# Kernel tuning notes

Hardware: AMD Instinct MI355X
Metric: run time of the kernel (lower is better)

Reference implementation:

```python
import jax, jax.numpy as jnp
import numpy as np

N_NODES = 50000
N_EDGES = 800000
IN_DIM, HID_DIM, OUT_DIM = 128, 128, 64


def setup_inputs() -> dict:
    key = jax.random.key(0)
    ks = jax.random.split(key, 12)
    x = jax.random.normal(ks[0], (N_NODES, IN_DIM), dtype=jnp.float32)
    src = jax.random.randint(ks[1], (N_EDGES,), 0, N_NODES, dtype=jnp.int32)
    dst = jax.random.randint(ks[2], (N_EDGES,), 0, N_NODES, dtype=jnp.int32)
    def lin(k, fan_in, fan_out):
        s = 1.0 / np.sqrt(fan_in)
        kw, kb = jax.random.split(k)
        W = jax.random.uniform(kw, (fan_in, fan_out), jnp.float32, -s, s)
        b = jax.random.uniform(kb, (fan_out,), jnp.float32, -s, s)
        return W, b
    W1, b1 = lin(ks[3], IN_DIM, HID_DIM)
    W2, b2 = lin(ks[4], HID_DIM, HID_DIM)
    W3, b3 = lin(ks[5], HID_DIM, OUT_DIM)
    Wf, bf = lin(ks[6], OUT_DIM, 1)
    return {"x": x, "src": src, "dst": dst,
            "W1": W1, "b1": b1, "W2": W2, "b2": b2,
            "W3": W3, "b3": b3, "Wf": Wf, "bf": bf}


def reference(x, src, dst, W1, b1, W2, b2, W3, b3, Wf, bf):
    n = x.shape[0]
    # GCN symmetric norm with self-loops: deg = in-degree + 1 (self loop)
    ones = jnp.ones(src.shape[0], x.dtype)
    deg = jax.ops.segment_sum(ones, dst, num_segments=n) + 1.0
    dinv = jax.lax.rsqrt(deg)                       # [N]
    edge_norm = dinv[src] * dinv[dst]               # [E]
    self_norm = dinv * dinv                         # [N], self-loop weight

    def gcn(h, W, b):
        h = h @ W                                   # transform first (PyG order)
        agg = jax.ops.segment_sum(h[src] * edge_norm[:, None], dst, num_segments=n)
        agg = agg + h * self_norm[:, None]          # self-loop contribution
        return agg + b

    h = jax.nn.relu(gcn(x, W1, b1))
    h = jax.nn.relu(gcn(h, W2, b2))
    h = jax.nn.relu(gcn(h, W3, b3))
    return h @ Wf + bf                              # [N, 1] per-node scores
```

## Files before the change

### kernel.cpp

```cpp
#include <hip/hip_runtime.h>
#include <hip/hip_bf16.h>

typedef short bf16x8 __attribute__((ext_vector_type(8)));
typedef float f32x4 __attribute__((ext_vector_type(4)));
typedef _Float16 f16x2 __attribute__((ext_vector_type(2)));
typedef _Float16 f16x8v __attribute__((ext_vector_type(8)));
typedef unsigned short u16x8 __attribute__((ext_vector_type(8)));

static __device__ __forceinline__ unsigned short f2bf_rne(float f) {
    unsigned int u = __float_as_uint(f);
    u += 0x7fff + ((u >> 16) & 1);
    return (unsigned short)(u >> 16);
}
static __device__ __forceinline__ float bf2f(unsigned short h) {
    return __uint_as_float(((unsigned int)h) << 16);
}

static __device__ __forceinline__ void wsplit_one(const float* W, unsigned short* hi,
                                                  unsigned short* lo, int BN, int idx) {
    int k = idx / BN, n = idx % BN;
    float w = W[idx];
    unsigned short h = f2bf_rne(w);
    unsigned short l = f2bf_rne(w - bf2f(h));
    int CT = BN >> 4;
    int kc = k >> 5, quad = (k >> 3) & 3, j = k & 7;
    int ct = n >> 4, c = n & 15;
    int slot = (((kc * CT + ct) * 4 + quad) * 16 + c) * 8 + j;
    hi[slot] = h;
    lo[slot] = l;
}


template<int BN>
static __device__ __forceinline__ void gemm_body_f32(const float* __restrict__ A,
                        const unsigned short* __restrict__ Whi, const unsigned short* __restrict__ Wlo,
                        _Float16* __restrict__ C, int N, int blk,
                        unsigned short* AhiS, unsigned short* AloS) {
    constexpr int CT = BN / 16;
    const int tid = threadIdx.x;
    const int wave = tid >> 6;
    const int lane = tid & 63;
    const int quad = lane >> 4;
    const int c16 = lane & 15;
    const int row0 = blk * 64;

    f32x4 acc[CT];
    #pragma unroll
    for (int t = 0; t < CT; ++t) acc[t] = (f32x4){0.f, 0.f, 0.f, 0.f};

    for (int kc = 0; kc < 4; ++kc) {
        #pragma unroll
        for (int r = 0; r < 2; ++r) {
            int f4 = tid + r * 256;
            int arow = f4 >> 3;
            int c4 = f4 & 7;
            int grow = row0 + arow;
            float4 v = make_float4(0.f, 0.f, 0.f, 0.f);
            if (grow < N) v = *(const float4*)&A[(size_t)grow * 128 + kc * 32 + c4 * 4];
            unsigned short h0 = f2bf_rne(v.x), h1 = f2bf_rne(v.y), h2 = f2bf_rne(v.z), h3 = f2bf_rne(v.w);
            ushort4 hv = make_ushort4(h0, h1, h2, h3);
            ushort4 lv = make_ushort4(f2bf_rne(v.x - bf2f(h0)), f2bf_rne(v.y - bf2f(h1)),
                                      f2bf_rne(v.z - bf2f(h2)), f2bf_rne(v.w - bf2f(h3)));
            int q = c4 >> 1;
            int joff = (c4 & 1) * 4;
            int base = (q * 64 + arow) * 8 + joff;
            *(ushort4*)&AhiS[base] = hv;
            *(ushort4*)&AloS[base] = lv;
        }
        __syncthreads();

        int abase = (quad * 64 + wave * 16 + c16) * 8;
        bf16x8 ahi = *(const bf16x8*)&AhiS[abase];
        bf16x8 alo = *(const bf16x8*)&AloS[abase];

        #pragma unroll
        for (int ct = 0; ct < CT; ++ct) {
            size_t bslot = ((size_t)(kc * CT + ct) * 64 + lane) * 8;
            bf16x8 bhi = *(const bf16x8*)&Whi[bslot];
            bf16x8 blo = *(const bf16x8*)&Wlo[bslot];
            acc[ct] = __builtin_amdgcn_mfma_f32_16x16x32_bf16(ahi, bhi, acc[ct], 0, 0, 0);
            acc[ct] = __builtin_amdgcn_mfma_f32_16x16x32_bf16(ahi, blo, acc[ct], 0, 0, 0);
            acc[ct] = __builtin_amdgcn_mfma_f32_16x16x32_bf16(alo, bhi, acc[ct], 0, 0, 0);
        }
        __syncthreads();
    }

    #pragma unroll
    for (int ct = 0; ct < CT; ++ct) {
        #pragma unroll
        for (int r = 0; r < 4; ++r) {
            int grow = row0 + wave * 16 + quad * 4 + r;
            if (grow < N) C[(size_t)grow * BN + ct * 16 + c16] = (_Float16)acc[ct][r];
        }
    }
}

template<int BN>
static __device__ __forceinline__ void gemm_body_bf(const unsigned short* __restrict__ Ahi,
                        const unsigned short* __restrict__ Alo,
                        const unsigned short* __restrict__ Whi, const unsigned short* __restrict__ Wlo,
                        _Float16* __restrict__ C, int N, int blk,
                        unsigned short* AhiS, unsigned short* AloS) {
    constexpr int CT = BN / 16;
    const int tid = threadIdx.x;
    const int wave = tid >> 6;
    const int lane = tid & 63;
    const int quad = lane >> 4;
    const int c16 = lane & 15;
    const int row0 = blk * 64;
    const int arow = tid >> 2;
    const int cblk = tid & 3;
    const int grow = row0 + arow;
    const bool inb = grow < N;
    const size_t agbase = (size_t)grow * 128 + cblk * 8;
    const int sbase = (cblk * 64 + arow) * 8;

    f32x4 acc[CT];
    #pragma unroll
    for (int t = 0; t < CT; ++t) acc[t] = (f32x4){0.f, 0.f, 0.f, 0.f};

    for (int kc = 0; kc < 4; ++kc) {
        u16x8 hv = {0, 0, 0, 0, 0, 0, 0, 0};
        u16x8 lv = {0, 0, 0, 0, 0, 0, 0, 0};
        if (inb) {
            hv = *(const u16x8*)&Ahi[agbase + kc * 32];
            lv = *(const u16x8*)&Alo[agbase + kc * 32];
        }
        *(u16x8*)&AhiS[sbase] = hv;
        *(u16x8*)&AloS[sbase] = lv;
        __syncthreads();

        int abase = (quad * 64 + wave * 16 + c16) * 8;
        bf16x8 ahi = *(const bf16x8*)&AhiS[abase];
        bf16x8 alo = *(const bf16x8*)&AloS[abase];

        #pragma unroll
        for (int ct = 0; ct < CT; ++ct) {
            size_t bslot = ((size_t)(kc * CT + ct) * 64 + lane) * 8;
            bf16x8 bhi = *(const bf16x8*)&Whi[bslot];
            bf16x8 blo = *(const bf16x8*)&Wlo[bslot];
            acc[ct] = __builtin_amdgcn_mfma_f32_16x16x32_bf16(ahi, bhi, acc[ct], 0, 0, 0);
            acc[ct] = __builtin_amdgcn_mfma_f32_16x16x32_bf16(ahi, blo, acc[ct], 0, 0, 0);
            acc[ct] = __builtin_amdgcn_mfma_f32_16x16x32_bf16(alo, bhi, acc[ct], 0, 0, 0);
        }
        __syncthreads();
    }

    #pragma unroll
    for (int ct = 0; ct < CT; ++ct) {
        #pragma unroll
        for (int r = 0; r < 4; ++r) {
            int gr = row0 + wave * 16 + quad * 4 + r;
            if (gr < N) C[(size_t)gr * BN + ct * 16 + c16] = (_Float16)acc[ct][r];
        }
    }
}


__global__ __launch_bounds__(256) void k_count_wsplit(const int* __restrict__ dst, int* __restrict__ deg,
                          int* __restrict__ rank,
                          const float* __restrict__ W1, const float* __restrict__ W2, const float* __restrict__ W3,
                          unsigned short* __restrict__ W1hi, unsigned short* __restrict__ W1lo,
                          unsigned short* __restrict__ W2hi, unsigned short* __restrict__ W2lo,
                          unsigned short* __restrict__ W3hi, unsigned short* __restrict__ W3lo,
                          int E) {
    int e = blockIdx.x * blockDim.x + threadIdx.x;
    if (e < E) rank[e] = atomicAdd(&deg[dst[e]], 1);
    if (e < 128 * 128) {
        wsplit_one(W1, W1hi, W1lo, 128, e);
        wsplit_one(W2, W2hi, W2lo, 128, e);
    }
    if (e < 128 * 64) wsplit_one(W3, W3hi, W3lo, 64, e);
}

__global__ __launch_bounds__(1024) void k_scan(const int* __restrict__ deg, float* __restrict__ dinv,
                                               int* __restrict__ row_start, int N) {
    __shared__ int s[1024];
    __shared__ int wsum[16];
    __shared__ int prefix;
    const int t = threadIdx.x;
    const int base = blockIdx.x * 1024;

    {
        int v = 0;
        for (int j = t; j < base; j += 1024) v += deg[j];
        for (int off = 32; off > 0; off >>= 1) v += __shfl_down(v, off, 64);
        if ((t & 63) == 0) wsum[t >> 6] = v;
        __syncthreads();
        if (t == 0) {
            int acc = 0;
            #pragma unroll
            for (int k = 0; k < 16; ++k) acc += wsum[k];
            prefix = acc;
        }
    }

    int i = base + t;
    int v = 0;
    if (i < N) {
        v = deg[i];
        dinv[i] = rsqrtf((float)v + 1.0f);
    }
    s[t] = v;
    __syncthreads();
    for (int off = 1; off < 1024; off <<= 1) {
        int x = (t >= off) ? s[t - off] : 0;
        __syncthreads();
        s[t] += x;
        __syncthreads();
    }
    if (i <= N) row_start[i] = prefix + s[t] - v;
}


__global__ __launch_bounds__(256, 2) void k_gemm1_scatter(const float* __restrict__ A,
                          const unsigned short* __restrict__ Whi, const unsigned short* __restrict__ Wlo,
                          _Float16* __restrict__ C, int N, int gemmGrid,
                          const int* __restrict__ src, const int* __restrict__ dst,
                          const int* __restrict__ row_start, const int* __restrict__ rank,
                          const float* __restrict__ dinv, int2* __restrict__ cv, int E) {
    __shared__ unsigned short AhiS[4 * 64 * 8];
    __shared__ unsigned short AloS[4 * 64 * 8];
    if ((int)blockIdx.x < gemmGrid) {
        gemm_body_f32<128>(A, Whi, Wlo, C, N, blockIdx.x, AhiS, AloS);
    } else {
        int e = (blockIdx.x - gemmGrid) * 256 + threadIdx.x;
        if (e < E) {
            int d = dst[e];
            int s = src[e];
            cv[row_start[d] + rank[e]] = make_int2(s, __float_as_int(dinv[s]));
        }
    }
}

template<int BN>
__global__ __launch_bounds__(256, 2) void k_gemm_bf(const unsigned short* __restrict__ Ahi,
                        const unsigned short* __restrict__ Alo,
                        const unsigned short* __restrict__ Whi, const unsigned short* __restrict__ Wlo,
                        _Float16* __restrict__ C, int N) {
    __shared__ unsigned short AhiS[4 * 64 * 8];
    __shared__ unsigned short AloS[4 * 64 * 8];
    gemm_body_bf<BN>(Ahi, Alo, Whi, Wlo, C, N, blockIdx.x, AhiS, AloS);
}


__global__ __launch_bounds__(256) void k_agg128(const _Float16* __restrict__ t,
                      unsigned short* __restrict__ outHi, unsigned short* __restrict__ outLo,
                      const int* __restrict__ row_start, const int2* __restrict__ cv,
                      const float* __restrict__ dinv, const float* __restrict__ bias,
                      int N) {
    int gid = blockIdx.x * blockDim.x + threadIdx.x;
    int node = gid >> 6;
    int lane = gid & 63;
    if (node >= N) return;
    int l16 = lane & 15;
    int g4 = lane >> 4;
    int p = row_start[node];
    int end = row_start[node + 1];
    const f16x8v* tp8 = (const f16x8v*)t;
    float a[8];
    #pragma unroll
    for (int d = 0; d < 8; ++d) a[d] = 0.f;

    while (p < end) {
        int idx = p + l16;
        int2 h = (idx < end) ? cv[idx] : make_int2(0, 0);
        #pragma unroll
        for (int jj = 0; jj < 4; ++jj) {
            int sl = jj * 4 + g4;
            int s = __shfl(h.x, sl, 64);
            float w = __int_as_float(__shfl(h.y, sl, 64));
            f16x8v v = tp8[(size_t)s * 16 + l16];
            #pragma unroll
            for (int d = 0; d < 8; ++d) a[d] += w * (float)v[d];
        }
        p += 16;
    }
    #pragma unroll
    for (int d = 0; d < 8; ++d) {
        a[d] += __shfl_xor(a[d], 16, 64);
        a[d] += __shfl_xor(a[d], 32, 64);
    }
    float di = dinv[node];
    f16x8v sv = tp8[(size_t)node * 16 + l16];
    float4 b0 = ((const float4*)bias)[l16 * 2];
    float4 b1 = ((const float4*)bias)[l16 * 2 + 1];
    float bb[8] = {b0.x, b0.y, b0.z, b0.w, b1.x, b1.y, b1.z, b1.w};
    u16x8 hw, lw;
    #pragma unroll
    for (int d = 0; d < 8; ++d) {
        float r = fmaxf(di * a[d] + di * di * (float)sv[d] + bb[d], 0.f);
        unsigned short hx = f2bf_rne(r);
        hw[d] = hx;
        lw[d] = f2bf_rne(r - bf2f(hx));
    }
    if (g4 == 0) {
        *(u16x8*)&outHi[(size_t)node * 128 + l16 * 8] = hw;
        *(u16x8*)&outLo[(size_t)node * 128 + l16 * 8] = lw;
    }
}

__global__ __launch_bounds__(256) void k_agg64_final(const _Float16* __restrict__ t, float* __restrict__ outp,
                      const int* __restrict__ row_start, const int2* __restrict__ cv,
                      const float* __restrict__ dinv, const float* __restrict__ bias,
                      const float* __restrict__ Wf, const float* __restrict__ bf,
                      int N) {
    int gid = blockIdx.x * blockDim.x + threadIdx.x;
    int node = gid >> 6;
    int lane = gid & 63;
    if (node >= N) return;
    int l8 = lane & 7;
    int g8 = lane >> 3;
    int p = row_start[node];
    int end = row_start[node + 1];
    const f16x8v* tp8 = (const f16x8v*)t;
    float a[8];
    #pragma unroll
    for (int d = 0; d < 8; ++d) a[d] = 0.f;

    while (p < end) {
        int idx = p + (lane & 15);
        int2 h = (idx < end) ? cv[idx] : make_int2(0, 0);
        #pragma unroll
        for (int jj = 0; jj < 2; ++jj) {
            int sl = jj * 8 + g8;
            int s = __shfl(h.x, sl, 64);
            float w = __int_as_float(__shfl(h.y, sl, 64));
            f16x8v v = tp8[(size_t)s * 8 + l8];
            #pragma unroll
            for (int d = 0; d < 8; ++d) a[d] += w * (float)v[d];
        }
        p += 16;
    }
    #pragma unroll
    for (int d = 0; d < 8; ++d) {
        a[d] += __shfl_xor(a[d], 8, 64);
        a[d] += __shfl_xor(a[d], 16, 64);
        a[d] += __shfl_xor(a[d], 32, 64);
    }
    float di = dinv[node];
    f16x8v sv = tp8[(size_t)node * 8 + l8];
    float4 b0 = ((const float4*)bias)[l8 * 2];
    float4 b1 = ((const float4*)bias)[l8 * 2 + 1];
    float bb[8] = {b0.x, b0.y, b0.z, b0.w, b1.x, b1.y, b1.z, b1.w};
    float4 w0 = ((const float4*)Wf)[l8 * 2];
    float4 w1 = ((const float4*)Wf)[l8 * 2 + 1];
    float ww[8] = {w0.x, w0.y, w0.z, w0.w, w1.x, w1.y, w1.z, w1.w};
    float dot = 0.f;
    #pragma unroll
    for (int d = 0; d < 8; ++d) {
        float r = fmaxf(di * a[d] + di * di * (float)sv[d] + bb[d], 0.f);
        dot += r * ww[d];
    }
    dot += __shfl_xor(dot, 1, 64);
    dot += __shfl_xor(dot, 2, 64);
    dot += __shfl_xor(dot, 4, 64);
    if (lane == 0) outp[node] = dot + bf[0];
}


extern "C" void kernel_launch(void* const* d_in, const int* in_sizes, int n_in,
                              void* d_out, int out_size, void* d_ws, size_t ws_size,
                              hipStream_t stream) {
    const float* x  = (const float*)d_in[0];
    const int*   src = (const int*)d_in[1];
    const int*   dst = (const int*)d_in[2];
    const float* W1 = (const float*)d_in[3];
    const float* b1 = (const float*)d_in[4];
    const float* W2 = (const float*)d_in[5];
    const float* b2 = (const float*)d_in[6];
    const float* W3 = (const float*)d_in[7];
    const float* b3 = (const float*)d_in[8];
    const float* Wf = (const float*)d_in[9];
    const float* bf = (const float*)d_in[10];
    float* out = (float*)d_out;

    const int N = 50000;
    const int E = 800000;

    char* ws = (char*)d_ws;
    size_t off = 0;
    auto alloc = [&](size_t bytes) -> void* {
        void* p = (void*)(ws + off);
        off += (bytes + 511) & ~((size_t)511);
        return p;
    };
    int*   deg       = (int*)alloc((size_t)N * 4);
    float* dinv      = (float*)alloc((size_t)N * 4);
    int*   row_start = (int*)alloc((size_t)(N + 1) * 4);
    int*   rank      = (int*)alloc((size_t)E * 4);
    int2*  cv        = (int2*)alloc((size_t)E * 8);
    _Float16* bufT   = (_Float16*)alloc((size_t)N * 128 * 2);
    unsigned short* bufHi = (unsigned short*)alloc((size_t)N * 128 * 2);
    unsigned short* bufLo = (unsigned short*)alloc((size_t)N * 128 * 2);
    unsigned short* W1hi = (unsigned short*)alloc(128 * 128 * 2);
    unsigned short* W1lo = (unsigned short*)alloc(128 * 128 * 2);
    unsigned short* W2hi = (unsigned short*)alloc(128 * 128 * 2);
    unsigned short* W2lo = (unsigned short*)alloc(128 * 128 * 2);
    unsigned short* W3hi = (unsigned short*)alloc(128 * 64 * 2);
    unsigned short* W3lo = (unsigned short*)alloc(128 * 64 * 2);

    hipMemsetAsync(deg, 0, (size_t)N * 4, stream);

    k_count_wsplit<<<(E + 255) / 256, 256, 0, stream>>>(dst, deg, rank, W1, W2, W3,
                                                        W1hi, W1lo, W2hi, W2lo, W3hi, W3lo, E);
    int NB = (N + 1023) / 1024;
    k_scan<<<NB, 1024, 0, stream>>>(deg, dinv, row_start, N);

    int gemmGrid = (N + 63) / 64;
    int scatGrid = (E + 255) / 256;
    int aggGrid = (N * 64 + 255) / 256;

    k_gemm1_scatter<<<gemmGrid + scatGrid, 256, 0, stream>>>(x, W1hi, W1lo, bufT, N, gemmGrid,
                                                             src, dst, row_start, rank, dinv, cv, E);
    k_agg128<<<aggGrid, 256, 0, stream>>>(bufT, bufHi, bufLo, row_start, cv, dinv, b1, N);
    k_gemm_bf<128><<<gemmGrid, 256, 0, stream>>>(bufHi, bufLo, W2hi, W2lo, bufT, N);
    k_agg128<<<aggGrid, 256, 0, stream>>>(bufT, bufHi, bufLo, row_start, cv, dinv, b2, N);
    k_gemm_bf<64><<<gemmGrid, 256, 0, stream>>>(bufHi, bufLo, W3hi, W3lo, bufT, N);
    k_agg64_final<<<aggGrid, 256, 0, stream>>>(bufT, out, row_start, cv, dinv, b3, Wf, bf, N);
}
```

Before: 275.1 us.

## Store hidden activations as fp16 and fill CSR via atomic cursors

The aggregation kernels now write post-ReLU activations as a single fp16 buffer, not separate bf16 hi/lo buffers, and the GEMM splits fp16 into hi/lo in registers on load. This halves activation write and read traffic between the aggregation and GEMM stages. The CSR build drops the per-edge rank array and places each edge with an atomicAdd on a per-node cursor, which removes the rank write and read but adds a second round of atomics and makes the edge order within each row nondeterministic. Storing activations in fp16 loses precision against the previous hi/lo bf16 pair.

```diff
diff --git a/kernel.cpp b/kernel.cpp
--- a/kernel.cpp
+++ b/kernel.cpp
@@ -96,8 +96,7 @@
 }
 
 template<int BN>
-static __device__ __forceinline__ void gemm_body_bf(const unsigned short* __restrict__ Ahi,
-                        const unsigned short* __restrict__ Alo,
+static __device__ __forceinline__ void gemm_body_f16src(const _Float16* __restrict__ A,
                         const unsigned short* __restrict__ Whi, const unsigned short* __restrict__ Wlo,
                         _Float16* __restrict__ C, int N, int blk,
                         unsigned short* AhiS, unsigned short* AloS) {
@@ -120,11 +119,15 @@
     for (int t = 0; t < CT; ++t) acc[t] = (f32x4){0.f, 0.f, 0.f, 0.f};
 
     for (int kc = 0; kc < 4; ++kc) {
-        u16x8 hv = {0, 0, 0, 0, 0, 0, 0, 0};
-        u16x8 lv = {0, 0, 0, 0, 0, 0, 0, 0};
-        if (inb) {
-            hv = *(const u16x8*)&Ahi[agbase + kc * 32];
-            lv = *(const u16x8*)&Alo[agbase + kc * 32];
+        f16x8v v = {0, 0, 0, 0, 0, 0, 0, 0};
+        if (inb) v = *(const f16x8v*)&A[agbase + kc * 32];
+        u16x8 hv, lv;
+        #pragma unroll
+        for (int d = 0; d < 8; ++d) {
+            float f = (float)v[d];
+            unsigned short h = f2bf_rne(f);
+            hv[d] = h;
+            lv[d] = f2bf_rne(f - bf2f(h));
         }
         *(u16x8*)&AhiS[sbase] = hv;
         *(u16x8*)&AloS[sbase] = lv;
@@ -158,14 +161,13 @@
 
 
 __global__ __launch_bounds__(256) void k_count_wsplit(const int* __restrict__ dst, int* __restrict__ deg,
-                          int* __restrict__ rank,
                           const float* __restrict__ W1, const float* __restrict__ W2, const float* __restrict__ W3,
                           unsigned short* __restrict__ W1hi, unsigned short* __restrict__ W1lo,
                           unsigned short* __restrict__ W2hi, unsigned short* __restrict__ W2lo,
                           unsigned short* __restrict__ W3hi, unsigned short* __restrict__ W3lo,
                           int E) {
     int e = blockIdx.x * blockDim.x + threadIdx.x;
-    if (e < E) rank[e] = atomicAdd(&deg[dst[e]], 1);
+    if (e < E) atomicAdd(&deg[dst[e]], 1);
     if (e < 128 * 128) {
         wsplit_one(W1, W1hi, W1lo, 128, e);
         wsplit_one(W2, W2hi, W2lo, 128, e);
@@ -174,7 +176,8 @@
 }
 
 __global__ __launch_bounds__(1024) void k_scan(const int* __restrict__ deg, float* __restrict__ dinv,
-                                               int* __restrict__ row_start, int N) {
+                                               int* __restrict__ row_start, int* __restrict__ cursor,
+                                               int N) {
     __shared__ int s[1024];
     __shared__ int wsum[16];
     __shared__ int prefix;
@@ -209,7 +212,11 @@
         s[t] += x;
         __syncthreads();
     }
-    if (i <= N) row_start[i] = prefix + s[t] - v;
+    if (i <= N) {
+        int rs = prefix + s[t] - v;
+        row_start[i] = rs;
+        if (i < N) cursor[i] = rs;
+    }
 }
 
 
@@ -217,7 +224,7 @@
                           const unsigned short* __restrict__ Whi, const unsigned short* __restrict__ Wlo,
                           _Float16* __restrict__ C, int N, int gemmGrid,
                           const int* __restrict__ src, const int* __restrict__ dst,
-                          const int* __restrict__ row_start, const int* __restrict__ rank,
+                          int* __restrict__ cursor,
                           const float* __restrict__ dinv, int2* __restrict__ cv, int E) {
     __shared__ unsigned short AhiS[4 * 64 * 8];
     __shared__ unsigned short AloS[4 * 64 * 8];
@@ -228,24 +235,24 @@
         if (e < E) {
             int d = dst[e];
             int s = src[e];
-            cv[row_start[d] + rank[e]] = make_int2(s, __float_as_int(dinv[s]));
+            int pos = atomicAdd(&cursor[d], 1);
+            cv[pos] = make_int2(s, __float_as_int(dinv[s]));
         }
     }
 }
 
 template<int BN>
-__global__ __launch_bounds__(256, 2) void k_gemm_bf(const unsigned short* __restrict__ Ahi,
-                        const unsigned short* __restrict__ Alo,
+__global__ __launch_bounds__(256, 2) void k_gemm_f16(const _Float16* __restrict__ A,
                         const unsigned short* __restrict__ Whi, const unsigned short* __restrict__ Wlo,
                         _Float16* __restrict__ C, int N) {
     __shared__ unsigned short AhiS[4 * 64 * 8];
     __shared__ unsigned short AloS[4 * 64 * 8];
-    gemm_body_bf<BN>(Ahi, Alo, Whi, Wlo, C, N, blockIdx.x, AhiS, AloS);
+    gemm_body_f16src<BN>(A, Whi, Wlo, C, N, blockIdx.x, AhiS, AloS);
 }
 
 
 __global__ __launch_bounds__(256) void k_agg128(const _Float16* __restrict__ t,
-                      unsigned short* __restrict__ outHi, unsigned short* __restrict__ outLo,
+                      _Float16* __restrict__ outA,
                       const int* __restrict__ row_start, const int2* __restrict__ cv,
                       const float* __restrict__ dinv, const float* __restrict__ bias,
                       int N) {
@@ -286,17 +293,14 @@
     float4 b0 = ((const float4*)bias)[l16 * 2];
     float4 b1 = ((const float4*)bias)[l16 * 2 + 1];
     float bb[8] = {b0.x, b0.y, b0.z, b0.w, b1.x, b1.y, b1.z, b1.w};
-    u16x8 hw, lw;
+    f16x8v hw;
     #pragma unroll
     for (int d = 0; d < 8; ++d) {
         float r = fmaxf(di * a[d] + di * di * (float)sv[d] + bb[d], 0.f);
-        unsigned short hx = f2bf_rne(r);
-        hw[d] = hx;
-        lw[d] = f2bf_rne(r - bf2f(hx));
+        hw[d] = (_Float16)r;
     }
     if (g4 == 0) {
-        *(u16x8*)&outHi[(size_t)node * 128 + l16 * 8] = hw;
-        *(u16x8*)&outLo[(size_t)node * 128 + l16 * 8] = lw;
+        *(f16x8v*)&outA[(size_t)node * 128 + l16 * 8] = hw;
     }
 }
 
@@ -388,11 +392,10 @@
     int*   deg       = (int*)alloc((size_t)N * 4);
     float* dinv      = (float*)alloc((size_t)N * 4);
     int*   row_start = (int*)alloc((size_t)(N + 1) * 4);
-    int*   rank      = (int*)alloc((size_t)E * 4);
+    int*   cursor    = (int*)alloc((size_t)N * 4);
     int2*  cv        = (int2*)alloc((size_t)E * 8);
     _Float16* bufT   = (_Float16*)alloc((size_t)N * 128 * 2);
-    unsigned short* bufHi = (unsigned short*)alloc((size_t)N * 128 * 2);
-    unsigned short* bufLo = (unsigned short*)alloc((size_t)N * 128 * 2);
+    _Float16* bufA   = (_Float16*)alloc((size_t)N * 128 * 2);
     unsigned short* W1hi = (unsigned short*)alloc(128 * 128 * 2);
     unsigned short* W1lo = (unsigned short*)alloc(128 * 128 * 2);
     unsigned short* W2hi = (unsigned short*)alloc(128 * 128 * 2);
@@ -402,20 +405,20 @@
 
     hipMemsetAsync(deg, 0, (size_t)N * 4, stream);
 
-    k_count_wsplit<<<(E + 255) / 256, 256, 0, stream>>>(dst, deg, rank, W1, W2, W3,
+    k_count_wsplit<<<(E + 255) / 256, 256, 0, stream>>>(dst, deg, W1, W2, W3,
                                                         W1hi, W1lo, W2hi, W2lo, W3hi, W3lo, E);
     int NB = (N + 1023) / 1024;
-    k_scan<<<NB, 1024, 0, stream>>>(deg, dinv, row_start, N);
+    k_scan<<<NB, 1024, 0, stream>>>(deg, dinv, row_start, cursor, N);
 
     int gemmGrid = (N + 63) / 64;
     int scatGrid = (E + 255) / 256;
     int aggGrid = (N * 64 + 255) / 256;
 
     k_gemm1_scatter<<<gemmGrid + scatGrid, 256, 0, stream>>>(x, W1hi, W1lo, bufT, N, gemmGrid,
-                                                             src, dst, row_start, rank, dinv, cv, E);
-    k_agg128<<<aggGrid, 256, 0, stream>>>(bufT, bufHi, bufLo, row_start, cv, dinv, b1, N);
-    k_gemm_bf<128><<<gemmGrid, 256, 0, stream>>>(bufHi, bufLo, W2hi, W2lo, bufT, N);
-    k_agg128<<<aggGrid, 256, 0, stream>>>(bufT, bufHi, bufLo, row_start, cv, dinv, b2, N);
-    k_gemm_bf<64><<<gemmGrid, 256, 0, stream>>>(bufHi, bufLo, W3hi, W3lo, bufT, N);
+                                                             src, dst, cursor, dinv, cv, E);
+    k_agg128<<<aggGrid, 256, 0, stream>>>(bufT, bufA, row_start, cv, dinv, b1, N);
+    k_gemm_f16<128><<<gemmGrid, 256, 0, stream>>>(bufA, W2hi, W2lo, bufT, N);
+    k_agg128<<<aggGrid, 256, 0, stream>>>(bufT, bufA, row_start, cv, dinv, b2, N);
+    k_gemm_f16<64><<<gemmGrid, 256, 0, stream>>>(bufA, W3hi, W3lo, bufT, N);
     k_agg64_final<<<aggGrid, 256, 0, stream>>>(bufT, out, row_start, cv, dinv, b3, Wf, bf, N);
 }
```

Result: slower. 299.1 us (+8.7%).
